# Kernel optimization log

Hardware: AMD Instinct MI355X
Metric: run time of the kernel (lower is better)

Reference implementation:

```python
import jax, jax.numpy as jnp
import numpy as np

N_NODES = 65536
N_EDGES = 1048576
BN_EPS = 1e-5


def _glorot(key, shape):
    fan_in, fan_out = shape[0], shape[1]
    lim = np.sqrt(6.0 / (fan_in + fan_out))
    return jax.random.uniform(key, shape, jnp.float32, -lim, lim)


def setup_inputs() -> dict:
    key = jax.random.key(0)
    ks = jax.random.split(key, 16)
    inp = {}
    inp['x'] = jax.random.normal(ks[0], (N_NODES, 3), jnp.float32)
    inp['edge_src'] = jax.random.randint(ks[1], (N_EDGES,), 0, N_NODES, jnp.int32)
    inp['edge_dst'] = jax.random.randint(ks[2], (N_EDGES,), 0, N_NODES, jnp.int32)
    inp['edge_val'] = jax.random.uniform(ks[3], (N_EDGES,), jnp.float32)
    inp['num_pts'] = 1024  # points per shape (equal-size split)
    # GraphConvolution params: out = adj @ (x @ W) + b
    inp['gc1_w'] = _glorot(ks[4], (3, 64));     inp['gc1_b'] = jnp.zeros((64,), jnp.float32)
    inp['gc2_w'] = _glorot(ks[5], (64, 64));    inp['gc2_b'] = jnp.zeros((64,), jnp.float32)
    inp['gc3_w'] = _glorot(ks[6], (64, 1024));  inp['gc3_b'] = jnp.zeros((1024,), jnp.float32)
    # MLP head: Linear(1024,512)+BN+ReLU, Linear(512,256)+BN+ReLU, Linear(256,40)
    inp['fc1_w'] = _glorot(ks[7], (1024, 512)); inp['fc1_b'] = jnp.zeros((512,), jnp.float32)
    inp['bn1_g'] = jnp.ones((512,), jnp.float32); inp['bn1_b'] = jnp.zeros((512,), jnp.float32)
    inp['fc2_w'] = _glorot(ks[8], (512, 256));  inp['fc2_b'] = jnp.zeros((256,), jnp.float32)
    inp['bn2_g'] = jnp.ones((256,), jnp.float32); inp['bn2_b'] = jnp.zeros((256,), jnp.float32)
    inp['fc3_w'] = _glorot(ks[9], (256, 40));   inp['fc3_b'] = jnp.zeros((40,), jnp.float32)
    return inp


def _gcn_layer(x, w, b, src, dst, val):
    # adj @ (x @ W) + b, adj given as COO edge list (dst <- src weighted by val)
    support = x @ w                                   # [N, F_out]
    msg = support[src] * val[:, None]                 # gather + scale
    agg = jax.ops.segment_sum(msg, dst, num_segments=N_NODES)
    return agg + b


def _batchnorm(x, gamma, beta):
    mean = jnp.mean(x, axis=0)
    var = jnp.mean(jnp.square(x - mean), axis=0)  # biased var (torch train mode)
    return (x - mean) * jax.lax.rsqrt(var + BN_EPS) * gamma + beta


def reference(x, edge_src, edge_dst, edge_val, num_pts,
              gc1_w, gc1_b, gc2_w, gc2_b, gc3_w, gc3_b,
              fc1_w, fc1_b, bn1_g, bn1_b, fc2_w, fc2_b, bn2_g, bn2_b, fc3_w, fc3_b):
    h = jax.nn.relu(_gcn_layer(x, gc1_w, gc1_b, edge_src, edge_dst, edge_val))
    h = jax.nn.relu(_gcn_layer(h, gc2_w, gc2_b, edge_src, edge_dst, edge_val))
    h = jax.nn.relu(_gcn_layer(h, gc3_w, gc3_b, edge_src, edge_dst, edge_val))
    # per-shape max pool: split into equal-size shapes along node dim
    n_shapes = N_NODES // num_pts
    global_feat = jnp.max(h.reshape(n_shapes, num_pts, 1024), axis=1)  # [B, 1024]
    # MLP head with train-mode BatchNorm
    z = jax.nn.relu(_batchnorm(global_feat @ fc1_w + fc1_b, bn1_g, bn1_b))
    z = jax.nn.relu(_batchnorm(z @ fc2_w + fc2_b, bn2_g, bn2_b))
    scores = z @ fc3_w + fc3_b                         # [B, 40]
    return jax.nn.log_softmax(scores, axis=-1)
```

## Files before the change

### kernel.cpp

```cpp
#include <hip/hip_runtime.h>
#include <math.h>

#define NN 65536
#define NE 1048576
#define CAP 17408
#define PCAP 24576

typedef __attribute__((ext_vector_type(8))) short short8;
typedef __attribute__((ext_vector_type(4))) float f32x4;

__device__ inline unsigned short f2bf(float f) {
  unsigned u = __float_as_uint(f);
  unsigned r = u + 0x7fff + ((u >> 16) & 1);
  return (unsigned short)(r >> 16);
}
__device__ inline float bf2f(unsigned short h) { return __uint_as_float(((unsigned)h) << 16); }

__global__ __launch_bounds__(256) void k_packx(const float* __restrict__ x, float4* __restrict__ x4,
                                               int* __restrict__ gcur) {
  int n = blockIdx.x * 256 + threadIdx.x;
  if (blockIdx.x == 0 && threadIdx.x < 64) gcur[threadIdx.x] = 0;
  x4[n] = make_float4(x[3 * n], x[3 * n + 1], x[3 * n + 2], 0.f);
}

__global__ __launch_bounds__(256) void k_bin(const int* __restrict__ src, const int* __restrict__ dst,
                                             const float* __restrict__ val, int* __restrict__ gcur,
                                             uint2* __restrict__ ebin) {
  __shared__ int cnt[64], base[64];
  int tid = threadIdx.x;
  if (tid < 64) cnt[tid] = 0;
  __syncthreads();
  int e0 = blockIdx.x * 4096;
  int rsrc[16], rdst[16], rrank[16];
  float rval[16];
#pragma unroll
  for (int i = 0; i < 16; ++i) {
    int e = e0 + i * 256 + tid;
    rsrc[i] = src[e];
    rdst[i] = dst[e];
    rval[i] = val[e];
    rrank[i] = atomicAdd(&cnt[rdst[i] >> 10], 1);
  }
  __syncthreads();
  if (tid < 64) base[tid] = atomicAdd(&gcur[tid], cnt[tid]);
  __syncthreads();
#pragma unroll
  for (int i = 0; i < 16; ++i) {
    int b = rdst[i] >> 10;
    ebin[b * CAP + base[b] + rrank[i]] =
        make_uint2((unsigned)rsrc[i] | ((unsigned)(rdst[i] & 1023) << 16), (unsigned)__float_as_int(rval[i]));
  }
}

__global__ __launch_bounds__(1024) void k_csr(const int* __restrict__ gcnt, const uint2* __restrict__ ebin,
                                              int2* __restrict__ offdeg, int2* __restrict__ pack) {
  __shared__ int lcnt[1024], lcur[1024], part[1024];
  int b = blockIdx.x, tid = threadIdx.x;
  int count = gcnt[b];
  int gbase = b * PCAP;
  lcnt[tid] = 0;
  __syncthreads();
  const uint2* eb = ebin + (size_t)b * CAP;
  for (int i0 = 0; i0 < count; i0 += 4096) {
    unsigned xs[4];
#pragma unroll
    for (int u = 0; u < 4; ++u) {
      int i = i0 + u * 1024 + tid;
      xs[u] = eb[min(i, count - 1)].x;
    }
#pragma unroll
    for (int u = 0; u < 4; ++u) {
      int i = i0 + u * 1024 + tid;
      if (i < count) atomicAdd(&lcnt[(xs[u] >> 16) & 1023], 1);
    }
  }
  __syncthreads();
  int deg = lcnt[tid];
  int pdeg = (deg + 7) & ~7;
  part[tid] = pdeg;
  __syncthreads();
  for (int d = 1; d < 1024; d <<= 1) {
    int v = (tid >= d) ? part[tid - d] : 0;
    __syncthreads();
    part[tid] += v;
    __syncthreads();
  }
  int o0 = part[tid] - pdeg;
  lcur[tid] = o0;
  offdeg[b * 1024 + tid] = make_int2(gbase + o0, pdeg);
  __syncthreads();
  for (int i0 = 0; i0 < count; i0 += 4096) {
    uint2 es[4];
#pragma unroll
    for (int u = 0; u < 4; ++u) {
      int i = i0 + u * 1024 + tid;
      es[u] = eb[min(i, count - 1)];
    }
#pragma unroll
    for (int u = 0; u < 4; ++u) {
      int i = i0 + u * 1024 + tid;
      if (i < count) {
        int ld = (es[u].x >> 16) & 1023;
        int p = atomicAdd(&lcur[ld], 1);
        pack[gbase + p] = make_int2((int)((es[u].x & 0xffffu) << 7), (int)es[u].y);
      }
    }
  }
  int pend = o0 + pdeg;
  for (int p = o0 + deg; p < pend; ++p) pack[gbase + p] = make_int2(0, 0);
}

__global__ __launch_bounds__(256) void k_aggx(const int2* __restrict__ offdeg, const int2* __restrict__ pack,
                                              const float4* __restrict__ x4, float* __restrict__ aggx) {
  int n = blockIdx.x * 256 + threadIdx.x;
  int2 od = offdeg[n];
  int i0 = od.x, pdeg = od.y;
  float a0 = 0.f, a1 = 0.f, a2 = 0.f;
  for (int b = 0; b < pdeg; b += 8) {
    int2 ed[8];
    float4 q[8];
#pragma unroll
    for (int u = 0; u < 8; ++u) ed[u] = pack[i0 + b + u];
#pragma unroll
    for (int u = 0; u < 8; ++u) q[u] = x4[(unsigned)ed[u].x >> 7];
#pragma unroll
    for (int u = 0; u < 8; ++u) {
      float v = __int_as_float(ed[u].y);
      a0 = fmaf(v, q[u].x, a0);
      a1 = fmaf(v, q[u].y, a1);
      a2 = fmaf(v, q[u].z, a2);
    }
  }
  aggx[n * 3 + 0] = a0;
  aggx[n * 3 + 1] = a1;
  aggx[n * 3 + 2] = a2;
}

__global__ __launch_bounds__(256) void k_gemm1(const float* __restrict__ aggx, const float* __restrict__ w,
                                               const float* __restrict__ b, unsigned short* __restrict__ out) {
  __shared__ float sw[256];
  int t = threadIdx.x;
  sw[t] = (t < 192) ? w[t] : b[t - 192];
  __syncthreads();
  int g = blockIdx.x * 256 + t;
  int n = g >> 6, j = g & 63;
  float a0 = aggx[n * 3], a1 = aggx[n * 3 + 1], a2 = aggx[n * 3 + 2];
  float r = sw[192 + j];
  r = fmaf(a0, sw[j], r);
  r = fmaf(a1, sw[64 + j], r);
  r = fmaf(a2, sw[128 + j], r);
  out[g] = f2bf(fmaxf(r, 0.f));
}

__global__ __launch_bounds__(256) void k_agg64g2(const int2* __restrict__ offdeg, const int2* __restrict__ pack,
                                                 const unsigned short* __restrict__ h,
                                                 const float* __restrict__ w2, const float* __restrict__ b2,
                                                 unsigned short* __restrict__ out) {
  __shared__ float sw[64][64];
  __shared__ float rows[16][64];
  int tid = threadIdx.x;
  int lane = tid & 63, wv = tid >> 6;
  for (int t = tid; t < 1024; t += 256) ((float4*)sw)[t] = ((const float4*)w2)[t];
  __syncthreads();
  int q = lane >> 4, fl = lane & 15;
  int n = blockIdx.x * 16 + wv * 4 + q;
  int2 od = offdeg[n];
  int i0 = od.x, pdeg = od.y;
  const char* hb = (const char*)h;
  unsigned fo = (unsigned)(fl << 3);
  float c0 = 0.f, c1 = 0.f, c2 = 0.f, c3 = 0.f;
  for (int b = 0; b < pdeg; b += 8) {
    int2 ed[8];
    uint2 hv[8];
#pragma unroll
    for (int u = 0; u < 8; ++u) ed[u] = pack[i0 + b + u];
#pragma unroll
    for (int u = 0; u < 8; ++u) hv[u] = *(const uint2*)(hb + ((unsigned)ed[u].x + fo));
#pragma unroll
    for (int u = 0; u < 8; ++u) {
      float v = __int_as_float(ed[u].y);
      c0 = fmaf(v, __uint_as_float(hv[u].x << 16), c0);
      c1 = fmaf(v, __uint_as_float(hv[u].x & 0xffff0000u), c1);
      c2 = fmaf(v, __uint_as_float(hv[u].y << 16), c2);
      c3 = fmaf(v, __uint_as_float(hv[u].y & 0xffff0000u), c3);
    }
  }
  ((float4*)rows[wv * 4 + q])[fl] = make_float4(c0, c1, c2, c3);
  int nA = blockIdx.x * 16 + wv * 4;
  float bb = b2[lane];
  float aA = bb, aB = bb, aC = bb, aD = bb;
  const float4* rA = (const float4*)rows[wv * 4 + 0];
  const float4* rB = (const float4*)rows[wv * 4 + 1];
  const float4* rC = (const float4*)rows[wv * 4 + 2];
  const float4* rD = (const float4*)rows[wv * 4 + 3];
#pragma unroll
  for (int kk = 0; kk < 16; ++kk) {
    float4 qa = rA[kk], qb = rB[kk], qc = rC[kk], qd = rD[kk];
    float w0 = sw[4 * kk + 0][lane], w1 = sw[4 * kk + 1][lane];
    float w2v = sw[4 * kk + 2][lane], w3v = sw[4 * kk + 3][lane];
    aA = fmaf(qa.x, w0, aA); aB = fmaf(qb.x, w0, aB); aC = fmaf(qc.x, w0, aC); aD = fmaf(qd.x, w0, aD);
    aA = fmaf(qa.y, w1, aA); aB = fmaf(qb.y, w1, aB); aC = fmaf(qc.y, w1, aC); aD = fmaf(qd.y, w1, aD);
    aA = fmaf(qa.z, w2v, aA); aB = fmaf(qb.z, w2v, aB); aC = fmaf(qc.z, w2v, aC); aD = fmaf(qd.z, w2v, aD);
    aA = fmaf(qa.w, w3v, aA); aB = fmaf(qb.w, w3v, aB); aC = fmaf(qc.w, w3v, aC); aD = fmaf(qd.w, w3v, aD);
  }
  out[(size_t)(nA + 0) * 64 + lane] = f2bf(fmaxf(aA, 0.f));
  out[(size_t)(nA + 1) * 64 + lane] = f2bf(fmaxf(aB, 0.f));
  out[(size_t)(nA + 2) * 64 + lane] = f2bf(fmaxf(aC, 0.f));
  out[(size_t)(nA + 3) * 64 + lane] = f2bf(fmaxf(aD, 0.f));
}

__global__ __launch_bounds__(256) void k_agg64_split(const int2* __restrict__ offdeg, const int2* __restrict__ pack,
                                                     const unsigned short* __restrict__ h,
                                                     unsigned short* __restrict__ hi,
                                                     unsigned short* __restrict__ lo) {
  int tid = threadIdx.x;
  int lane = tid & 63, wv = tid >> 6;
  int q = lane >> 4, fl = lane & 15;
  int n = blockIdx.x * 16 + wv * 4 + q;
  int2 od = offdeg[n];
  int i0 = od.x, pdeg = od.y;
  const char* hb = (const char*)h;
  unsigned fo = (unsigned)(fl << 3);
  float c0 = 0.f, c1 = 0.f, c2 = 0.f, c3 = 0.f;
  for (int b = 0; b < pdeg; b += 8) {
    int2 ed[8];
    uint2 hv[8];
#pragma unroll
    for (int u = 0; u < 8; ++u) ed[u] = pack[i0 + b + u];
#pragma unroll
    for (int u = 0; u < 8; ++u) hv[u] = *(const uint2*)(hb + ((unsigned)ed[u].x + fo));
#pragma unroll
    for (int u = 0; u < 8; ++u) {
      float v = __int_as_float(ed[u].y);
      c0 = fmaf(v, __uint_as_float(hv[u].x << 16), c0);
      c1 = fmaf(v, __uint_as_float(hv[u].x & 0xffff0000u), c1);
      c2 = fmaf(v, __uint_as_float(hv[u].y << 16), c2);
      c3 = fmaf(v, __uint_as_float(hv[u].y & 0xffff0000u), c3);
    }
  }
  unsigned short h0 = f2bf(c0), h1 = f2bf(c1), h2 = f2bf(c2), h3 = f2bf(c3);
  unsigned short l0 = f2bf(c0 - bf2f(h0)), l1 = f2bf(c1 - bf2f(h1));
  unsigned short l2 = f2bf(c2 - bf2f(h2)), l3 = f2bf(c3 - bf2f(h3));
  ((uint2*)hi)[(size_t)n * 16 + fl] = make_uint2((unsigned)h0 | ((unsigned)h1 << 16), (unsigned)h2 | ((unsigned)h3 << 16));
  ((uint2*)lo)[(size_t)n * 16 + fl] = make_uint2((unsigned)l0 | ((unsigned)l1 << 16), (unsigned)l2 | ((unsigned)l3 << 16));
}

__global__ __launch_bounds__(256) void k_prepw(const float* __restrict__ w3, unsigned short* __restrict__ bfrag,
                                               unsigned* __restrict__ gf) {
  int t = blockIdx.x * 256 + threadIdx.x;
  if (t < 65536) gf[t] = 0u;
  int e = t & 7, g = (t >> 3) & 3, col = (t >> 5) & 1023, q = t >> 15;
  int k = (q & 1) * 32 + g * 8 + e;
  float v = w3[k * 1024 + col];
  unsigned short hv = f2bf(v);
  bfrag[t] = (q < 2) ? hv : f2bf(v - bf2f(hv));
}

__global__ __launch_bounds__(512) void k_gemm3max(const unsigned short* __restrict__ Ahi,
                                                  const unsigned short* __restrict__ Alo,
                                                  const unsigned short* __restrict__ Bfrag,
                                                  const float* __restrict__ b3,
                                                  unsigned* __restrict__ gf) {
  int b = blockIdx.x;
  int colhalf = b & 1, rowchunk = b >> 1;
  int shape = rowchunk >> 2;
  int tid = threadIdx.x;
  int wv = tid >> 6, l = tid & 63;
  int g = l >> 4, lr = l & 15;

  const short8* bf = (const short8*)Bfrag;
  int c0 = colhalf * 512 + wv * 64 + lr;
  short8 B0[4], B1[4], B2[4], B3[4];
#pragma unroll
  for (int ct = 0; ct < 4; ++ct) {
    int col = c0 + ct * 16;
    B0[ct] = bf[(0 * 1024 + col) * 4 + g];
    B1[ct] = bf[(1 * 1024 + col) * 4 + g];
    B2[ct] = bf[(2 * 1024 + col) * 4 + g];
    B3[ct] = bf[(3 * 1024 + col) * 4 + g];
  }

  float m[4] = {-1e30f, -1e30f, -1e30f, -1e30f};
  size_t abase = ((size_t)rowchunk * 256 + lr) * 64 + g * 8;
  for (int t = 0; t < 16; ++t) {
    size_t o = abase + (size_t)t * 16 * 64;
    short8 ah0 = *(const short8*)(Ahi + o);
    short8 ah1 = *(const short8*)(Ahi + o + 32);
    short8 al0 = *(const short8*)(Alo + o);
    short8 al1 = *(const short8*)(Alo + o + 32);
#pragma unroll
    for (int ct = 0; ct < 4; ++ct) {
      f32x4 acc = {0.f, 0.f, 0.f, 0.f};
      acc = __builtin_amdgcn_mfma_f32_16x16x32_bf16(ah0, B0[ct], acc, 0, 0, 0);
      acc = __builtin_amdgcn_mfma_f32_16x16x32_bf16(ah1, B1[ct], acc, 0, 0, 0);
      acc = __builtin_amdgcn_mfma_f32_16x16x32_bf16(ah0, B2[ct], acc, 0, 0, 0);
      acc = __builtin_amdgcn_mfma_f32_16x16x32_bf16(ah1, B3[ct], acc, 0, 0, 0);
      acc = __builtin_amdgcn_mfma_f32_16x16x32_bf16(al0, B0[ct], acc, 0, 0, 0);
      acc = __builtin_amdgcn_mfma_f32_16x16x32_bf16(al1, B1[ct], acc, 0, 0, 0);
      m[ct] = fmaxf(m[ct], fmaxf(fmaxf(acc[0], acc[1]), fmaxf(acc[2], acc[3])));
    }
  }
#pragma unroll
  for (int ct = 0; ct < 4; ++ct) {
    float mm = m[ct];
    mm = fmaxf(mm, __shfl_xor(mm, 16));
    mm = fmaxf(mm, __shfl_xor(mm, 32));
    if (g == 0) {
      int col = c0 + ct * 16;
      float v = fmaxf(mm + b3[col], 0.f);
      atomicMax(&gf[shape * 1024 + col], __float_as_uint(v));
    }
  }
}

__global__ __launch_bounds__(512) void k_fc(const float* __restrict__ in, const float* __restrict__ w,
                                            const float* __restrict__ bias, float* __restrict__ out,
                                            int K, int J) {
  __shared__ float sin_[1024];
  __shared__ float part[8][64];
  int jt = blockIdx.x, bb = blockIdx.y;
  int tid = threadIdx.x, s = tid >> 6, lane = tid & 63;
  for (int i = tid; i < K; i += 512) sin_[i] = in[bb * K + i];
  __syncthreads();
  int j = (jt << 6) + lane;
  int Ks = K >> 3;
  int k0 = s * Ks;
  float acc = 0.f;
  for (int k = 0; k < Ks; k += 16) {
    float wv[16];
#pragma unroll
    for (int u = 0; u < 16; ++u) wv[u] = w[(k0 + k + u) * J + j];
#pragma unroll
    for (int u = 0; u < 16; ++u) acc = fmaf(sin_[k0 + k + u], wv[u], acc);
  }
  part[s][lane] = acc;
  __syncthreads();
  if (tid < 64) {
    float r = bias[(jt << 6) + tid];
#pragma unroll
    for (int u = 0; u < 8; ++u) r += part[u][tid];
    out[bb * J + (jt << 6) + tid] = r;
  }
}

__global__ __launch_bounds__(256) void k_bn(const float* __restrict__ z, const float* __restrict__ g,
                                            const float* __restrict__ bt, float* __restrict__ out, int J) {
  __shared__ float tile[64][64];
  __shared__ float red[4][64];
  __shared__ float sc[64], sh[64];
  int tid = threadIdx.x, s = tid >> 6, lane = tid & 63;
  int j0 = blockIdx.x << 6;
  float psum = 0.f;
#pragma unroll
  for (int r = 0; r < 16; ++r) {
    int row = s * 16 + r;
    float v = z[row * J + j0 + lane];
    tile[row][lane] = v;
    psum += v;
  }
  red[s][lane] = psum;
  __syncthreads();
  if (tid < 64) sc[tid] = (red[0][tid] + red[1][tid] + red[2][tid] + red[3][tid]) * (1.f / 64.f);
  __syncthreads();
  float mean = sc[lane];
  float pv = 0.f;
#pragma unroll
  for (int r = 0; r < 16; ++r) {
    float d = tile[s * 16 + r][lane] - mean;
    pv = fmaf(d, d, pv);
  }
  red[s][lane] = pv;
  __syncthreads();
  if (tid < 64) {
    float var = (red[0][tid] + red[1][tid] + red[2][tid] + red[3][tid]) * (1.f / 64.f);
    float scale = g[j0 + tid] / sqrtf(var + 1e-5f);
    sh[tid] = bt[j0 + tid] - sc[tid] * scale;
    sc[tid] = scale;
  }
  __syncthreads();
  float scale = sc[lane], shift = sh[lane];
#pragma unroll
  for (int r = 0; r < 16; ++r) {
    int row = s * 16 + r;
    out[row * J + j0 + lane] = fmaxf(fmaf(tile[row][lane], scale, shift), 0.f);
  }
}

__global__ __launch_bounds__(256) void k_head(const float* __restrict__ z, const float* __restrict__ w,
                                              const float* __restrict__ b, float* __restrict__ out) {
  __shared__ float sz[256];
  __shared__ float part[4][64];
  int bb = blockIdx.x, tid = threadIdx.x;
  sz[tid] = z[bb * 256 + tid];
  __syncthreads();
  int s = tid >> 6, j = tid & 63;
  float acc = 0.f;
  if (j < 40) {
#pragma unroll
    for (int k = 0; k < 64; k += 4) {
      int kk = s * 64 + k;
      acc = fmaf(sz[kk + 0], w[(kk + 0) * 40 + j], acc);
      acc = fmaf(sz[kk + 1], w[(kk + 1) * 40 + j], acc);
      acc = fmaf(sz[kk + 2], w[(kk + 2) * 40 + j], acc);
      acc = fmaf(sz[kk + 3], w[(kk + 3) * 40 + j], acc);
    }
  }
  part[s][j] = acc;
  __syncthreads();
  if (tid < 64) {
    float v = (j < 40) ? part[0][j] + part[1][j] + part[2][j] + part[3][j] + b[j] : -INFINITY;
    float m = v;
    for (int d = 32; d > 0; d >>= 1) m = fmaxf(m, __shfl_xor(m, d));
    float e = (j < 40) ? expf(v - m) : 0.f;
    for (int d = 32; d > 0; d >>= 1) e += __shfl_xor(e, d);
    if (j < 40) out[bb * 40 + j] = v - m - logf(e);
  }
}

extern "C" void kernel_launch(void* const* d_in, const int* in_sizes, int n_in,
                              void* d_out, int out_size, void* d_ws, size_t ws_size,
                              hipStream_t stream) {
  (void)in_sizes; (void)n_in; (void)out_size; (void)ws_size;
  const float* x    = (const float*)d_in[0];
  const int*   esrc = (const int*)d_in[1];
  const int*   edst = (const int*)d_in[2];
  const float* ev   = (const float*)d_in[3];
  const float* gc1w = (const float*)d_in[5];
  const float* gc1b = (const float*)d_in[6];
  const float* gc2w = (const float*)d_in[7];
  const float* gc2b = (const float*)d_in[8];
  const float* gc3w = (const float*)d_in[9];
  const float* gc3b = (const float*)d_in[10];
  const float* fc1w = (const float*)d_in[11];
  const float* fc1b = (const float*)d_in[12];
  const float* bn1g = (const float*)d_in[13];
  const float* bn1b = (const float*)d_in[14];
  const float* fc2w = (const float*)d_in[15];
  const float* fc2b = (const float*)d_in[16];
  const float* bn2g = (const float*)d_in[17];
  const float* bn2b = (const float*)d_in[18];
  const float* fc3w = (const float*)d_in[19];
  const float* fc3b = (const float*)d_in[20];

  char* ws = (char*)d_ws;
  size_t o = 0;
  auto alloc = [&](size_t bytes) -> void* {
    void* p = ws + o;
    o += (bytes + 255) & ~(size_t)255;
    return p;
  };
  int2*  offdeg = (int2*)alloc((size_t)NN * 8);
  int*   gcur = (int*)alloc(64 * 4);
  int2*  pack = (int2*)alloc((size_t)64 * PCAP * 8);
  float* aggx = (float*)alloc((size_t)NN * 3 * 4);
  float4* x4  = (float4*)alloc((size_t)NN * 16);
  float* bufA = (float*)alloc((size_t)NN * 64 * 4);
  float* bufB = (float*)alloc((size_t)NN * 64 * 4);
  uint2* ebin = (uint2*)bufA;
  unsigned short* h1_16 = (unsigned short*)bufA;
  unsigned short* h2_16 = (unsigned short*)((char*)bufA + NN * 64 * 2);
  unsigned short* Ahi = (unsigned short*)bufB;
  unsigned short* Alo = (unsigned short*)(bufB + NN * 32);
  unsigned short* Bfrag = (unsigned short*)alloc(4 * 1024 * 32 * 2);
  float* gf   = (float*)alloc(64 * 1024 * 4);
  float* z1   = (float*)alloc(64 * 512 * 4);
  float* z1n  = (float*)alloc(64 * 512 * 4);
  float* z2   = (float*)alloc(64 * 256 * 4);
  float* z2n  = (float*)alloc(64 * 256 * 4);

  k_packx<<<NN / 256, 256, 0, stream>>>(x, x4, gcur);
  k_prepw<<<512, 256, 0, stream>>>(gc3w, Bfrag, (unsigned*)gf);

  k_bin<<<NE / 4096, 256, 0, stream>>>(esrc, edst, ev, gcur, ebin);
  k_csr<<<64, 1024, 0, stream>>>(gcur, ebin, offdeg, pack);

  k_aggx<<<NN / 256, 256, 0, stream>>>(offdeg, pack, x4, aggx);
  k_gemm1<<<(NN * 64) / 256, 256, 0, stream>>>(aggx, gc1w, gc1b, h1_16);

  k_agg64g2<<<NN / 16, 256, 0, stream>>>(offdeg, pack, h1_16, gc2w, gc2b, h2_16);

  k_agg64_split<<<NN / 16, 256, 0, stream>>>(offdeg, pack, h2_16, Ahi, Alo);
  k_gemm3max<<<512, 512, 0, stream>>>(Ahi, Alo, Bfrag, gc3b, (unsigned*)gf);

  k_fc<<<dim3(8, 64), 512, 0, stream>>>(gf, fc1w, fc1b, z1, 1024, 512);
  k_bn<<<8, 256, 0, stream>>>(z1, bn1g, bn1b, z1n, 512);
  k_fc<<<dim3(4, 64), 512, 0, stream>>>(z1n, fc2w, fc2b, z2, 512, 256);
  k_bn<<<4, 256, 0, stream>>>(z2, bn2g, bn2b, z2n, 256);
  k_head<<<64, 256, 0, stream>>>(z2n, fc3w, fc3b, (float*)d_out);
}
```

Baseline: 171.9 us.

## Merge prep kernels, fuse BN2 into head, widen aggregation gathers to 16 bytes

Combines the input-packing and weight-prep kernels into one launch, and folds the second batchnorm into the head kernel, which recomputes the column statistics in every block. The two 64-wide aggregation kernels now have each lane load 8 bf16 features (16 bytes) per neighbor, so 8 lanes cover a node and each wave handles 8 nodes instead of 4. This halves the block count and doubles the per-thread accumulator and register load. The aim is fewer launches and wider gather loads, at the cost of redundant BN statistic work and higher register pressure in the gather kernels.

```diff
diff --git a/kernel.cpp b/kernel.cpp
--- a/kernel.cpp
+++ b/kernel.cpp
@@ -16,11 +16,23 @@
 }
 __device__ inline float bf2f(unsigned short h) { return __uint_as_float(((unsigned)h) << 16); }
 
-__global__ __launch_bounds__(256) void k_packx(const float* __restrict__ x, float4* __restrict__ x4,
-                                               int* __restrict__ gcur) {
-  int n = blockIdx.x * 256 + threadIdx.x;
-  if (blockIdx.x == 0 && threadIdx.x < 64) gcur[threadIdx.x] = 0;
-  x4[n] = make_float4(x[3 * n], x[3 * n + 1], x[3 * n + 2], 0.f);
+__global__ __launch_bounds__(256) void k_prep(const float* __restrict__ x, float4* __restrict__ x4,
+                                              int* __restrict__ gcur, const float* __restrict__ w3,
+                                              unsigned short* __restrict__ bfrag, unsigned* __restrict__ gf) {
+  int bid = blockIdx.x, tid = threadIdx.x;
+  if (bid < 256) {
+    if (bid == 0 && tid < 64) gcur[tid] = 0;
+    int n = bid * 256 + tid;
+    x4[n] = make_float4(x[3 * n], x[3 * n + 1], x[3 * n + 2], 0.f);
+  } else {
+    int t = (bid - 256) * 256 + tid;
+    if (t < 65536) gf[t] = 0u;
+    int e = t & 7, g = (t >> 3) & 3, col = (t >> 5) & 1023, q = t >> 15;
+    int k = (q & 1) * 32 + g * 8 + e;
+    float v = w3[k * 1024 + col];
+    unsigned short hv = f2bf(v);
+    bfrag[t] = (q < 2) ? hv : f2bf(v - bf2f(hv));
+  }
 }
 
 __global__ __launch_bounds__(256) void k_bin(const int* __restrict__ src, const int* __restrict__ dst,
@@ -157,25 +169,25 @@
                                                  const float* __restrict__ w2, const float* __restrict__ b2,
                                                  unsigned short* __restrict__ out) {
   __shared__ float sw[64][64];
-  __shared__ float rows[16][64];
+  __shared__ float rows[32][64];
   int tid = threadIdx.x;
   int lane = tid & 63, wv = tid >> 6;
   for (int t = tid; t < 1024; t += 256) ((float4*)sw)[t] = ((const float4*)w2)[t];
   __syncthreads();
-  int q = lane >> 4, fl = lane & 15;
-  int n = blockIdx.x * 16 + wv * 4 + q;
+  int o = lane >> 3, fl = lane & 7;
+  int n = blockIdx.x * 32 + wv * 8 + o;
   int2 od = offdeg[n];
   int i0 = od.x, pdeg = od.y;
   const char* hb = (const char*)h;
-  unsigned fo = (unsigned)(fl << 3);
-  float c0 = 0.f, c1 = 0.f, c2 = 0.f, c3 = 0.f;
+  unsigned fo = (unsigned)(fl << 4);
+  float c0 = 0.f, c1 = 0.f, c2 = 0.f, c3 = 0.f, c4 = 0.f, c5 = 0.f, c6 = 0.f, c7 = 0.f;
   for (int b = 0; b < pdeg; b += 8) {
     int2 ed[8];
-    uint2 hv[8];
+    uint4 hv[8];
 #pragma unroll
     for (int u = 0; u < 8; ++u) ed[u] = pack[i0 + b + u];
 #pragma unroll
-    for (int u = 0; u < 8; ++u) hv[u] = *(const uint2*)(hb + ((unsigned)ed[u].x + fo));
+    for (int u = 0; u < 8; ++u) hv[u] = *(const uint4*)(hb + ((unsigned)ed[u].x + fo));
 #pragma unroll
     for (int u = 0; u < 8; ++u) {
       float v = __int_as_float(ed[u].y);
@@ -183,30 +195,35 @@
       c1 = fmaf(v, __uint_as_float(hv[u].x & 0xffff0000u), c1);
       c2 = fmaf(v, __uint_as_float(hv[u].y << 16), c2);
       c3 = fmaf(v, __uint_as_float(hv[u].y & 0xffff0000u), c3);
-    }
-  }
-  ((float4*)rows[wv * 4 + q])[fl] = make_float4(c0, c1, c2, c3);
-  int nA = blockIdx.x * 16 + wv * 4;
+      c4 = fmaf(v, __uint_as_float(hv[u].z << 16), c4);
+      c5 = fmaf(v, __uint_as_float(hv[u].z & 0xffff0000u), c5);
+      c6 = fmaf(v, __uint_as_float(hv[u].w << 16), c6);
+      c7 = fmaf(v, __uint_as_float(hv[u].w & 0xffff0000u), c7);
+    }
+  }
+  ((float4*)rows[wv * 8 + o])[fl * 2 + 0] = make_float4(c0, c1, c2, c3);
+  ((float4*)rows[wv * 8 + o])[fl * 2 + 1] = make_float4(c4, c5, c6, c7);
+  int nA = blockIdx.x * 32 + wv * 8;
   float bb = b2[lane];
-  float aA = bb, aB = bb, aC = bb, aD = bb;
-  const float4* rA = (const float4*)rows[wv * 4 + 0];
-  const float4* rB = (const float4*)rows[wv * 4 + 1];
-  const float4* rC = (const float4*)rows[wv * 4 + 2];
-  const float4* rD = (const float4*)rows[wv * 4 + 3];
+  float acc[8];
+#pragma unroll
+  for (int r = 0; r < 8; ++r) acc[r] = bb;
 #pragma unroll
   for (int kk = 0; kk < 16; ++kk) {
-    float4 qa = rA[kk], qb = rB[kk], qc = rC[kk], qd = rD[kk];
     float w0 = sw[4 * kk + 0][lane], w1 = sw[4 * kk + 1][lane];
     float w2v = sw[4 * kk + 2][lane], w3v = sw[4 * kk + 3][lane];
-    aA = fmaf(qa.x, w0, aA); aB = fmaf(qb.x, w0, aB); aC = fmaf(qc.x, w0, aC); aD = fmaf(qd.x, w0, aD);
-    aA = fmaf(qa.y, w1, aA); aB = fmaf(qb.y, w1, aB); aC = fmaf(qc.y, w1, aC); aD = fmaf(qd.y, w1, aD);
-    aA = fmaf(qa.z, w2v, aA); aB = fmaf(qb.z, w2v, aB); aC = fmaf(qc.z, w2v, aC); aD = fmaf(qd.z, w2v, aD);
-    aA = fmaf(qa.w, w3v, aA); aB = fmaf(qb.w, w3v, aB); aC = fmaf(qc.w, w3v, aC); aD = fmaf(qd.w, w3v, aD);
-  }
-  out[(size_t)(nA + 0) * 64 + lane] = f2bf(fmaxf(aA, 0.f));
-  out[(size_t)(nA + 1) * 64 + lane] = f2bf(fmaxf(aB, 0.f));
-  out[(size_t)(nA + 2) * 64 + lane] = f2bf(fmaxf(aC, 0.f));
-  out[(size_t)(nA + 3) * 64 + lane] = f2bf(fmaxf(aD, 0.f));
+#pragma unroll
+    for (int r = 0; r < 8; ++r) {
+      float4 qr = ((const float4*)rows[wv * 8 + r])[kk];
+      acc[r] = fmaf(qr.x, w0, acc[r]);
+      acc[r] = fmaf(qr.y, w1, acc[r]);
+      acc[r] = fmaf(qr.z, w2v, acc[r]);
+      acc[r] = fmaf(qr.w, w3v, acc[r]);
+    }
+  }
+#pragma unroll
+  for (int r = 0; r < 8; ++r)
+    out[(size_t)(nA + r) * 64 + lane] = f2bf(fmaxf(acc[r], 0.f));
 }
 
 __global__ __launch_bounds__(256) void k_agg64_split(const int2* __restrict__ offdeg, const int2* __restrict__ pack,
@@ -215,20 +232,20 @@
                                                      unsigned short* __restrict__ lo) {
   int tid = threadIdx.x;
   int lane = tid & 63, wv = tid >> 6;
-  int q = lane >> 4, fl = lane & 15;
-  int n = blockIdx.x * 16 + wv * 4 + q;
+  int o = lane >> 3, fl = lane & 7;
+  int n = blockIdx.x * 32 + wv * 8 + o;
   int2 od = offdeg[n];
   int i0 = od.x, pdeg = od.y;
   const char* hb = (const char*)h;
-  unsigned fo = (unsigned)(fl << 3);
-  float c0 = 0.f, c1 = 0.f, c2 = 0.f, c3 = 0.f;
+  unsigned fo = (unsigned)(fl << 4);
+  float c0 = 0.f, c1 = 0.f, c2 = 0.f, c3 = 0.f, c4 = 0.f, c5 = 0.f, c6 = 0.f, c7 = 0.f;
   for (int b = 0; b < pdeg; b += 8) {
     int2 ed[8];
-    uint2 hv[8];
+    uint4 hv[8];
 #pragma unroll
     for (int u = 0; u < 8; ++u) ed[u] = pack[i0 + b + u];
 #pragma unroll
-    for (int u = 0; u < 8; ++u) hv[u] = *(const uint2*)(hb + ((unsigned)ed[u].x + fo));
+    for (int u = 0; u < 8; ++u) hv[u] = *(const uint4*)(hb + ((unsigned)ed[u].x + fo));
 #pragma unroll
     for (int u = 0; u < 8; ++u) {
       float v = __int_as_float(ed[u].y);
@@ -236,24 +253,24 @@
       c1 = fmaf(v, __uint_as_float(hv[u].x & 0xffff0000u), c1);
       c2 = fmaf(v, __uint_as_float(hv[u].y << 16), c2);
       c3 = fmaf(v, __uint_as_float(hv[u].y & 0xffff0000u), c3);
+      c4 = fmaf(v, __uint_as_float(hv[u].z << 16), c4);
+      c5 = fmaf(v, __uint_as_float(hv[u].z & 0xffff0000u), c5);
+      c6 = fmaf(v, __uint_as_float(hv[u].w << 16), c6);
+      c7 = fmaf(v, __uint_as_float(hv[u].w & 0xffff0000u), c7);
     }
   }
   unsigned short h0 = f2bf(c0), h1 = f2bf(c1), h2 = f2bf(c2), h3 = f2bf(c3);
+  unsigned short h4 = f2bf(c4), h5 = f2bf(c5), h6 = f2bf(c6), h7 = f2bf(c7);
+  uint4 hiw = make_uint4((unsigned)h0 | ((unsigned)h1 << 16), (unsigned)h2 | ((unsigned)h3 << 16),
+                         (unsigned)h4 | ((unsigned)h5 << 16), (unsigned)h6 | ((unsigned)h7 << 16));
   unsigned short l0 = f2bf(c0 - bf2f(h0)), l1 = f2bf(c1 - bf2f(h1));
   unsigned short l2 = f2bf(c2 - bf2f(h2)), l3 = f2bf(c3 - bf2f(h3));
-  ((uint2*)hi)[(size_t)n * 16 + fl] = make_uint2((unsigned)h0 | ((unsigned)h1 << 16), (unsigned)h2 | ((unsigned)h3 << 16));
-  ((uint2*)lo)[(size_t)n * 16 + fl] = make_uint2((unsigned)l0 | ((unsigned)l1 << 16), (unsigned)l2 | ((unsigned)l3 << 16));
-}
-
-__global__ __launch_bounds__(256) void k_prepw(const float* __restrict__ w3, unsigned short* __restrict__ bfrag,
-                                               unsigned* __restrict__ gf) {
-  int t = blockIdx.x * 256 + threadIdx.x;
-  if (t < 65536) gf[t] = 0u;
-  int e = t & 7, g = (t >> 3) & 3, col = (t >> 5) & 1023, q = t >> 15;
-  int k = (q & 1) * 32 + g * 8 + e;
-  float v = w3[k * 1024 + col];
-  unsigned short hv = f2bf(v);
-  bfrag[t] = (q < 2) ? hv : f2bf(v - bf2f(hv));
+  unsigned short l4 = f2bf(c4 - bf2f(h4)), l5 = f2bf(c5 - bf2f(h5));
+  unsigned short l6 = f2bf(c6 - bf2f(h6)), l7 = f2bf(c7 - bf2f(h7));
+  uint4 low = make_uint4((unsigned)l0 | ((unsigned)l1 << 16), (unsigned)l2 | ((unsigned)l3 << 16),
+                         (unsigned)l4 | ((unsigned)l5 << 16), (unsigned)l6 | ((unsigned)l7 << 16));
+  ((uint4*)hi)[(size_t)n * 8 + fl] = hiw;
+  ((uint4*)lo)[(size_t)n * 8 + fl] = low;
 }
 
 __global__ __launch_bounds__(512) void k_gemm3max(const unsigned short* __restrict__ Ahi,
@@ -386,34 +403,47 @@
   }
 }
 
-__global__ __launch_bounds__(256) void k_head(const float* __restrict__ z, const float* __restrict__ w,
-                                              const float* __restrict__ b, float* __restrict__ out) {
+__global__ __launch_bounds__(256) void k_head2(const float* __restrict__ z2, const float* __restrict__ g,
+                                               const float* __restrict__ bt, const float* __restrict__ w,
+                                               const float* __restrict__ b, float* __restrict__ out) {
   __shared__ float sz[256];
   __shared__ float part[4][64];
-  int bb = blockIdx.x, tid = threadIdx.x;
-  sz[tid] = z[bb * 256 + tid];
-  __syncthreads();
-  int s = tid >> 6, j = tid & 63;
+  int bb = blockIdx.x, j = threadIdx.x;
+  float s = 0.f;
+#pragma unroll 8
+  for (int r = 0; r < 64; ++r) s += z2[r * 256 + j];
+  float mean = s * (1.f / 64.f);
+  float v = 0.f;
+#pragma unroll 8
+  for (int r = 0; r < 64; ++r) {
+    float d = z2[r * 256 + j] - mean;
+    v = fmaf(d, d, v);
+  }
+  float scale = g[j] / sqrtf(v * (1.f / 64.f) + 1e-5f);
+  float shift = bt[j] - mean * scale;
+  sz[j] = fmaxf(fmaf(z2[bb * 256 + j], scale, shift), 0.f);
+  __syncthreads();
+  int sgrp = j >> 6, lane = j & 63;
   float acc = 0.f;
-  if (j < 40) {
+  if (lane < 40) {
 #pragma unroll
     for (int k = 0; k < 64; k += 4) {
-      int kk = s * 64 + k;
-      acc = fmaf(sz[kk + 0], w[(kk + 0) * 40 + j], acc);
-      acc = fmaf(sz[kk + 1], w[(kk + 1) * 40 + j], acc);
-      acc = fmaf(sz[kk + 2], w[(kk + 2) * 40 + j], acc);
-      acc = fmaf(sz[kk + 3], w[(kk + 3) * 40 + j], acc);
-    }
-  }
-  part[s][j] = acc;
-  __syncthreads();
-  if (tid < 64) {
-    float v = (j < 40) ? part[0][j] + part[1][j] + part[2][j] + part[3][j] + b[j] : -INFINITY;
-    float m = v;
+      int kk = sgrp * 64 + k;
+      acc = fmaf(sz[kk + 0], w[(kk + 0) * 40 + lane], acc);
+      acc = fmaf(sz[kk + 1], w[(kk + 1) * 40 + lane], acc);
+      acc = fmaf(sz[kk + 2], w[(kk + 2) * 40 + lane], acc);
+      acc = fmaf(sz[kk + 3], w[(kk + 3) * 40 + lane], acc);
+    }
+  }
+  part[sgrp][lane] = acc;
+  __syncthreads();
+  if (j < 64) {
+    float lv = (j < 40) ? part[0][j] + part[1][j] + part[2][j] + part[3][j] + b[j] : -INFINITY;
+    float m = lv;
     for (int d = 32; d > 0; d >>= 1) m = fmaxf(m, __shfl_xor(m, d));
-    float e = (j < 40) ? expf(v - m) : 0.f;
+    float e = (j < 40) ? expf(lv - m) : 0.f;
     for (int d = 32; d > 0; d >>= 1) e += __shfl_xor(e, d);
-    if (j < 40) out[bb * 40 + j] = v - m - logf(e);
+    if (j < 40) out[bb * 40 + j] = lv - m - logf(e);
   }
 }
 
@@ -466,10 +496,8 @@
   float* z1   = (float*)alloc(64 * 512 * 4);
   float* z1n  = (float*)alloc(64 * 512 * 4);
   float* z2   = (float*)alloc(64 * 256 * 4);
-  float* z2n  = (float*)alloc(64 * 256 * 4);
-
-  k_packx<<<NN / 256, 256, 0, stream>>>(x, x4, gcur);
-  k_prepw<<<512, 256, 0, stream>>>(gc3w, Bfrag, (unsigned*)gf);
+
+  k_prep<<<768, 256, 0, stream>>>(x, x4, gcur, gc3w, Bfrag, (unsigned*)gf);
 
   k_bin<<<NE / 4096, 256, 0, stream>>>(esrc, edst, ev, gcur, ebin);
   k_csr<<<64, 1024, 0, stream>>>(gcur, ebin, offdeg, pack);
@@ -477,14 +505,13 @@
   k_aggx<<<NN / 256, 256, 0, stream>>>(offdeg, pack, x4, aggx);
   k_gemm1<<<(NN * 64) / 256, 256, 0, stream>>>(aggx, gc1w, gc1b, h1_16);
 
-  k_agg64g2<<<NN / 16, 256, 0, stream>>>(offdeg, pack, h1_16, gc2w, gc2b, h2_16);
-
-  k_agg64_split<<<NN / 16, 256, 0, stream>>>(offdeg, pack, h2_16, Ahi, Alo);
+  k_agg64g2<<<NN / 32, 256, 0, stream>>>(offdeg, pack, h1_16, gc2w, gc2b, h2_16);
+
+  k_agg64_split<<<NN / 32, 256, 0, stream>>>(offdeg, pack, h2_16, Ahi, Alo);
   k_gemm3max<<<512, 512, 0, stream>>>(Ahi, Alo, Bfrag, gc3b, (unsigned*)gf);
 
   k_fc<<<dim3(8, 64), 512, 0, stream>>>(gf, fc1w, fc1b, z1, 1024, 512);
   k_bn<<<8, 256, 0, stream>>>(z1, bn1g, bn1b, z1n, 512);
   k_fc<<<dim3(4, 64), 512, 0, stream>>>(z1n, fc2w, fc2b, z2, 512, 256);
-  k_bn<<<4, 256, 0, stream>>>(z2, bn2g, bn2b, z2n, 256);
-  k_head<<<64, 256, 0, stream>>>(z2n, fc3w, fc3b, (float*)d_out);
-}
+  k_head2<<<64, 256, 0, stream>>>(z2, bn2g, bn2b, fc3w, fc3b, (float*)d_out);
+}
```

Measured after the change: 167.2 us. 1.03x faster.
